# Kernel tuning notes

Hardware: AMD Instinct MI355X
Metric: run time of the kernel (lower is better)

Reference implementation:

```python
import jax, jax.numpy as jnp
import numpy as np

B = 65536; D1 = 64; D2 = 64; DC = 128; K = 8; DFF = 1024
NPP = 3 * K - 1                      # 23 params per output dim (non-adaptive)
MIN_BIN = 0.1; MIN_DERIV = 1e-3; ALPHA = 2.0
DEFAULT = 3.0; DL = -DEFAULT; DD = 2 * DEFAULT; MIN_DELTA = MIN_BIN * K
SHIFT = float(np.log(np.e - 1.0))
SHIFT_DX = float(np.log(np.exp(DD - MIN_DELTA) - 1.0))
EPS = 1e-6


def setup_inputs() -> dict:
    key = jax.random.key(0)
    ks = jax.random.split(key, 8)
    x1 = jax.random.normal(ks[0], (B, D1), dtype=jnp.float32)
    x2 = jax.random.normal(ks[1], (B, D2), dtype=jnp.float32)
    context = jax.random.normal(ks[2], (B, DC), dtype=jnp.float32)
    mask1 = jnp.ones((B, D1), dtype=jnp.float32)
    din = 2 * D1 + DC
    W0 = jax.random.normal(ks[3], (din, DFF), dtype=jnp.float32) / np.sqrt(din)
    b0 = jnp.zeros((DFF,), jnp.float32)
    W1 = jax.random.normal(ks[4], (DFF, DFF), dtype=jnp.float32) / np.sqrt(DFF)
    b1 = jnp.zeros((DFF,), jnp.float32)
    W2 = jax.random.normal(ks[5], (DFF, DFF), dtype=jnp.float32) / np.sqrt(DFF)
    b2 = jnp.zeros((DFF,), jnp.float32)
    W3 = jax.random.normal(ks[6], (DFF, NPP * D2), dtype=jnp.float32) / np.sqrt(DFF)
    b3 = jnp.zeros((NPP * D2,), jnp.float32)
    return dict(x1=x1, x2=x2, context=context, mask1=mask1,
                W0=W0, b0=b0, W1=W1, b1=b1, W2=W2, b2=b2, W3=W3, b3=b3)


def _rq_forward(x1, x2, context, mask1, W0, b0, W1, b1, W2, b2, W3, b3):
    # --- conditioner MLP: input = concat(x1, mask1, context) ---
    h = jnp.concatenate([x1, mask1, context], axis=-1)
    h = jax.nn.relu(h @ W0 + b0)
    h = jax.nn.relu(h @ W1 + b1)
    h = jax.nn.relu(h @ W2 + b2)
    params = (h @ W3 + b3).reshape(x1.shape[0], D2, NPP)  # [B, D2, 23]

    w_raw = params[..., :K]
    h_raw = params[..., K:2 * K]
    d_raw = params[..., 2 * K:3 * K - 1]
    zeros = jnp.zeros(params.shape[:-1] + (1,), params.dtype)  # non-adaptive raw params

    # --- _constrain ---
    log_weight = ALPHA * jnp.tanh(zeros / ALPHA)          # -> 0
    weight = jnp.exp(log_weight)                          # -> 1
    bias = ALPHA * jnp.tanh(zeros / ALPHA)                # -> 0
    derivs = MIN_DERIV + jax.nn.softplus(d_raw + SHIFT)
    derivs = jnp.concatenate([weight, derivs, weight], axis=-1)  # [B, D2, K+1]
    left = DL + DD * jnp.tanh(zeros / DD)                 # -> -3
    delta_x = MIN_DELTA + jax.nn.softplus(zeros + SHIFT_DX)
    right = left + delta_x                                # -> +3
    bottom = weight * left + bias
    top = weight * right + bias

    w = jax.nn.softmax(w_raw, axis=-1)
    w = MIN_BIN + (1.0 - MIN_BIN * K) * w
    cw = jnp.pad(jnp.cumsum(w, axis=-1), ((0, 0), (0, 0), (1, 0)))
    cw = (right - left) * cw + left                       # cumwidths [B, D2, K+1]
    hh = jax.nn.softmax(h_raw, axis=-1)
    hh = MIN_BIN + (1.0 - MIN_BIN * K) * hh
    ch = jnp.pad(jnp.cumsum(hh, axis=-1), ((0, 0), (0, 0), (1, 0)))
    ch = (top - bottom) * ch + bottom                     # cumheights [B, D2, K+1]

    widths = cw[..., 1:] - cw[..., :-1]
    heights = ch[..., 1:] - ch[..., :-1]

    # --- bin search (searchsorted right=True on bumped cumwidths) ---
    bumped = jnp.concatenate([cw[..., :-1], cw[..., -1:] + EPS], axis=-1)
    idx = jnp.clip(jnp.sum(bumped <= x2[..., None], axis=-1) - 1, 0, K - 1)[..., None]

    gat = lambda t: jnp.take_along_axis(t, idx, axis=-1)[..., 0]
    x_k = gat(cw); x_kd = gat(widths)
    y_k = gat(ch); y_kd = gat(heights)
    s_k = gat(heights / widths)
    d0 = gat(derivs); d1 = gat(derivs[..., 1:])

    # --- forward rational-quadratic spline ---
    xi = (x2 - x_k) / x_kd
    xi1m = xi * (1.0 - xi)
    alpha_k = y_kd * (s_k * xi ** 2 + d0 * xi1m)
    beta_k = s_k + (d1 + d0 - 2.0 * s_k) * xi1m
    z_sp = y_k + alpha_k / jnp.maximum(beta_k, 1e-8)
    num = s_k ** 2 * (d1 * xi ** 2 + 2.0 * s_k * xi1m + d0 * (1.0 - xi) ** 2)
    ld_sp = jnp.log(jnp.maximum(num, 1e-8)) - 2.0 * jnp.log(jnp.maximum(beta_k, 1e-8))

    # --- affine tails ---
    lw = log_weight[..., 0]; bs = bias[..., 0]
    z_af = jnp.exp(lw) * x2 + bs
    ld_af = jnp.broadcast_to(lw, x2.shape)

    l2 = jnp.broadcast_to(left[..., 0], x2.shape)
    r2 = jnp.broadcast_to(right[..., 0], x2.shape)
    inside = (l2 <= x2) & (x2 < r2)
    z2 = jnp.where(inside, z_sp, z_af)
    ld = jnp.where(inside, ld_sp, ld_af)
    return z2, ld.sum(-1)


def reference(x1, x2, context, mask1, W0, b0, W1, b1, W2, b2, W3, b3):
    return _rq_forward(x1, x2, context, mask1, W0, b0, W1, b1, W2, b2, W3, b3)
```

## Files before the change

kernel.cpp:

```cpp
#include <hip/hip_runtime.h>


typedef __bf16 bf16_t;
typedef __bf16 bf16x8 __attribute__((ext_vector_type(8)));
typedef float f32x4 __attribute__((ext_vector_type(4)));

#define GLOAD_LDS16(g, l)                                               \
  __builtin_amdgcn_global_load_lds(                                     \
      (const __attribute__((address_space(1))) void*)(g),               \
      (__attribute__((address_space(3))) void*)(l), 16, 0, 0)

__device__ __forceinline__ void xcd_remap(int& bx, int& by) {
  const int gx = gridDim.x;
  const int nwg = gx * gridDim.y;
  const int id = blockIdx.y * gx + blockIdx.x;
  const int nid = (id & 7) * (nwg >> 3) + (id >> 3);
  bx = nid % gx;
  by = nid / gx;
}

__global__ __launch_bounds__(256) void transpose_w(
    const float* __restrict__ W, bf16_t* __restrict__ Wt,
    int K, int N, int Npad) {
  __shared__ float tile[64][65];
  const int kt = blockIdx.x * 64;
  const int nt = blockIdx.y * 64;
  const int r4 = threadIdx.x >> 6;
  const int c = threadIdx.x & 63;
#pragma unroll
  for (int i = 0; i < 16; i++) {
    int r = i * 4 + r4;
    int gn = nt + c;
    tile[r][c] = (gn < N) ? W[(size_t)(kt + r) * N + gn] : 0.0f;
  }
  __syncthreads();
#pragma unroll
  for (int i = 0; i < 16; i++) {
    int r = i * 4 + r4;
    Wt[(size_t)(nt + r) * K + kt + c] = (bf16_t)tile[c][r];
  }
}

__global__ __launch_bounds__(256) void transpose_w3p(
    const float* __restrict__ W3, bf16_t* __restrict__ Wt) {
  __shared__ float tile[64][65];
  const int kt = blockIdx.x * 64;
  const int nt = blockIdx.y * 64;
  const int r4 = threadIdx.x >> 6;
  const int c = threadIdx.x & 63;
  const int np = nt + c;
  const int d = np / 24, p = np % 24;
#pragma unroll
  for (int i = 0; i < 16; i++) {
    int r = i * 4 + r4;
    tile[r][c] = (p < 23) ? W3[(size_t)(kt + r) * 1472 + d * 23 + p] : 0.0f;
  }
  __syncthreads();
#pragma unroll
  for (int i = 0; i < 16; i++) {
    int r = i * 4 + r4;
    Wt[(size_t)(nt + r) * 1024 + kt + c] = (bf16_t)tile[c][r];
  }
}

__global__ __launch_bounds__(256) void prep_b3(const float* __restrict__ b3,
                                               float* __restrict__ b3p) {
  int t = blockIdx.x * 256 + threadIdx.x;
  if (t < 1536) {
    int d = t / 24, p = t % 24;
    b3p[t] = (p < 23) ? b3[d * 23 + p] : 0.0f;
  }
}

__global__ __launch_bounds__(256) void build_x(
    const float* __restrict__ x1, const float* __restrict__ mask1,
    const float* __restrict__ ctx, bf16_t* __restrict__ X,
    float* __restrict__ ld_out, int boff) {
  int idx = blockIdx.x * 256 + threadIdx.x;
  int bl = idx >> 8;
  int c = idx & 255;
  size_t b = (size_t)(boff + bl);
  float v;
  if (c < 64)       v = x1[b * 64 + c];
  else if (c < 128) v = mask1[b * 64 + (c - 64)];
  else              v = ctx[b * 128 + (c - 128)];
  X[(size_t)bl * 256 + c] = (bf16_t)v;
  if (c == 0) ld_out[b] = 0.0f;
}

__global__ __launch_bounds__(512, 4) void gemm_bt(
    const bf16_t* __restrict__ A, const bf16_t* __restrict__ Bt,
    const float* __restrict__ bias, bf16_t* __restrict__ Cout, int N, int K) {
  __shared__ __align__(16) bf16_t As[2][128 * 32];
  __shared__ __align__(16) bf16_t Bs[2][256 * 32];
  const int tid = threadIdx.x;
  const int w = tid >> 6;
  const int lane = tid & 63;
  int bx, by;
  xcd_remap(bx, by);
  const int m0 = by * 128;
  const int n0 = bx * 256;
  const int wm = (w & 1) * 64;
  const int wn = (w >> 1) * 64;
  const int lrow = lane & 15;
  const int quad = lane >> 4;

  const bf16_t* gA;
  {
    const int byteoff = (w << 10) + lane * 16;
    const int row = byteoff >> 6;
    const int qs = ((byteoff >> 4) & 3) ^ ((row >> 1) & 3);
    gA = A + (size_t)(m0 + row) * K + qs * 8;
  }
  const bf16_t* gB0;
  const bf16_t* gB1;
  {
    int byteoff = (w << 10) + lane * 16;
    int row = byteoff >> 6;
    int qs = ((byteoff >> 4) & 3) ^ ((row >> 1) & 3);
    gB0 = Bt + (size_t)(n0 + row) * K + qs * 8;
    byteoff = ((w + 8) << 10) + lane * 16;
    row = byteoff >> 6;
    qs = ((byteoff >> 4) & 3) ^ ((row >> 1) & 3);
    gB1 = Bt + (size_t)(n0 + row) * K + qs * 8;
  }
  bf16_t* const dA0 = &As[0][0] + w * 512;
  bf16_t* const dB0 = &Bs[0][0] + w * 512;
  bf16_t* const dB1 = &Bs[0][0] + (w + 8) * 512;

  int offA[4], offB[4];
#pragma unroll
  for (int i = 0; i < 4; i++) {
    const int rowA = wm + i * 16 + lrow;
    offA[i] = rowA * 32 + (quad ^ ((rowA >> 1) & 3)) * 8;
    const int rowB = wn + i * 16 + lrow;
    offB[i] = rowB * 32 + (quad ^ ((rowB >> 1) & 3)) * 8;
  }

  f32x4 acc[4][4];
#pragma unroll
  for (int i = 0; i < 4; i++)
#pragma unroll
    for (int j = 0; j < 4; j++) acc[i][j] = (f32x4){0.f, 0.f, 0.f, 0.f};

  const int nPair = K >> 6;
  for (int kp = 0; kp < nPair; kp++) {
    GLOAD_LDS16(gA, dA0);
    GLOAD_LDS16(gA + 32, dA0 + 4096);
    GLOAD_LDS16(gB0, dB0);
    GLOAD_LDS16(gB0 + 32, dB0 + 8192);
    GLOAD_LDS16(gB1, dB1);
    GLOAD_LDS16(gB1 + 32, dB1 + 8192);
    gA += 64;
    gB0 += 64;
    gB1 += 64;
    __syncthreads();
#pragma unroll
    for (int h = 0; h < 2; h++) {
      bf16x8 af[4], bfr[4];
#pragma unroll
      for (int i = 0; i < 4; i++)
        af[i] = *(const bf16x8*)(&As[0][0] + h * 4096 + offA[i]);
#pragma unroll
      for (int j = 0; j < 4; j++)
        bfr[j] = *(const bf16x8*)(&Bs[0][0] + h * 8192 + offB[j]);
#pragma unroll
      for (int i = 0; i < 4; i++)
#pragma unroll
        for (int j = 0; j < 4; j++)
          acc[i][j] = __builtin_amdgcn_mfma_f32_16x16x32_bf16(
              af[i], bfr[j], acc[i][j], 0, 0, 0);
    }
    __syncthreads();
  }

  float bv[4];
#pragma unroll
  for (int j = 0; j < 4; j++) bv[j] = bias[n0 + wn + j * 16 + lrow];
#pragma unroll
  for (int i = 0; i < 4; i++) {
    int rbase = m0 + wm + i * 16 + quad * 4;
#pragma unroll
    for (int j = 0; j < 4; j++) {
      int col = n0 + wn + j * 16 + lrow;
#pragma unroll
      for (int r = 0; r < 4; r++) {
        float v = fmaxf(acc[i][j][r] + bv[j], 0.0f);
        Cout[(size_t)(rbase + r) * N + col] = (bf16_t)v;
      }
    }
  }
}

__global__ __launch_bounds__(512, 4) void gemm_rq_fused(
    const bf16_t* __restrict__ A, const bf16_t* __restrict__ Bt,
    const float* __restrict__ b3p, const float* __restrict__ x2,
    float* __restrict__ z_out, float* __restrict__ ld_out,
    int boff, int K) {
  union alignas(16) SM {
    struct { bf16_t As[2][128 * 32]; bf16_t Bs[2][192 * 32]; } s;
    bf16_t Pt[128 * 200];
  };
  __shared__ SM sm;
  const int tid = threadIdx.x;
  const int w = tid >> 6;
  const int lane = tid & 63;
  int bx, by;
  xcd_remap(bx, by);
  const int m0 = by * 128;
  const int n0 = bx * 192;
  const int wm = (w & 1) * 64;
  const int wn = (w >> 1) * 48;
  const int lrow = lane & 15;
  const int quad = lane >> 4;

  bf16_t* const smB = &sm.s.As[0][0];

  const bf16_t* gA;
  {
    const int byteoff = (w << 10) + lane * 16;
    const int row = byteoff >> 6;
    const int qs = ((byteoff >> 4) & 3) ^ ((row >> 1) & 3);
    gA = A + (size_t)(m0 + row) * K + qs * 8;
  }
  const bf16_t* gB0;
  const bf16_t* gB1;
  {
    int byteoff = (w << 10) + lane * 16;
    int row = byteoff >> 6;
    int qs = ((byteoff >> 4) & 3) ^ ((row >> 1) & 3);
    gB0 = Bt + (size_t)(n0 + row) * K + qs * 8;
    const int c1 = (w & 3) + 8;
    byteoff = (c1 << 10) + lane * 16;
    row = byteoff >> 6;
    qs = ((byteoff >> 4) & 3) ^ ((row >> 1) & 3);
    gB1 = Bt + (size_t)(n0 + row) * K + qs * 8;
  }
  bf16_t* const dA0 = smB + w * 512;
  bf16_t* const dB0 = smB + 8192 + w * 512;
  bf16_t* const dB1 = smB + 8192 + ((w & 3) + 8) * 512;

  int offA[4], offB3[3];
#pragma unroll
  for (int i = 0; i < 4; i++) {
    const int rowA = wm + i * 16 + lrow;
    offA[i] = rowA * 32 + (quad ^ ((rowA >> 1) & 3)) * 8;
  }
#pragma unroll
  for (int j = 0; j < 3; j++) {
    const int rowB = wn + j * 16 + lrow;
    offB3[j] = rowB * 32 + (quad ^ ((rowB >> 1) & 3)) * 8;
  }

  f32x4 acc[4][3];
#pragma unroll
  for (int i = 0; i < 4; i++)
#pragma unroll
    for (int j = 0; j < 3; j++) acc[i][j] = (f32x4){0.f, 0.f, 0.f, 0.f};

  const int nPair = K >> 6;
  for (int kp = 0; kp < nPair; kp++) {
    GLOAD_LDS16(gA, dA0);
    GLOAD_LDS16(gA + 32, dA0 + 4096);
    GLOAD_LDS16(gB0, dB0);
    GLOAD_LDS16(gB0 + 32, dB0 + 6144);
    if (w < 4) {
      GLOAD_LDS16(gB1, dB1);
      GLOAD_LDS16(gB1 + 32, dB1 + 6144);
      gB1 += 64;
    }
    gA += 64;
    gB0 += 64;
    __syncthreads();
#pragma unroll
    for (int h = 0; h < 2; h++) {
      bf16x8 af[4], bfr[3];
#pragma unroll
      for (int i = 0; i < 4; i++)
        af[i] = *(const bf16x8*)(smB + h * 4096 + offA[i]);
#pragma unroll
      for (int j = 0; j < 3; j++)
        bfr[j] = *(const bf16x8*)(smB + 8192 + h * 6144 + offB3[j]);
#pragma unroll
      for (int i = 0; i < 4; i++)
#pragma unroll
        for (int j = 0; j < 3; j++)
          acc[i][j] = __builtin_amdgcn_mfma_f32_16x16x32_bf16(
              af[i], bfr[j], acc[i][j], 0, 0, 0);
    }
    __syncthreads();
  }

  float bv[3];
#pragma unroll
  for (int j = 0; j < 3; j++) bv[j] = b3p[n0 + wn + j * 16 + lrow];
#pragma unroll
  for (int i = 0; i < 4; i++) {
    const int rbase = wm + i * 16 + quad * 4;
#pragma unroll
    for (int j = 0; j < 3; j++) {
      const int col = wn + j * 16 + lrow;
#pragma unroll
      for (int r = 0; r < 4; r++)
        sm.Pt[(rbase + r) * 200 + col] = (bf16_t)(acc[i][j][r] + bv[j]);
    }
  }
  __syncthreads();

  const float SHIFT = 0.54132485f;
  const float SHIFT_DX = 5.1944682f;
  const float left = -3.0f;
  const float delta_x = 0.8f + log1pf(expf(SHIFT_DX));
  const float right = left + delta_x;
  const float scale = delta_x;
  const int dloc = tid & 7;
  const int dg = bx * 8 + dloc;

#pragma unroll
  for (int rr = 0; rr < 2; rr++) {
    const int row = (tid >> 3) + rr * 64;
    const bf16_t* pr = sm.Pt + row * 200 + dloc * 24;
    const size_t bg = (size_t)(boff + m0 + row);
    const float x = x2[bg * 64 + dg];

    bf16x8 v0 = *(const bf16x8*)(pr);
    bf16x8 v1 = *(const bf16x8*)(pr + 8);
    bf16x8 v2 = *(const bf16x8*)(pr + 16);
    float pv[24];
#pragma unroll
    for (int j = 0; j < 8; j++) pv[j] = (float)v0[j];
#pragma unroll
    for (int j = 0; j < 8; j++) pv[8 + j] = (float)v1[j];
#pragma unroll
    for (int j = 0; j < 8; j++) pv[16 + j] = (float)v2[j];

    float mw = pv[0];
#pragma unroll
    for (int j = 1; j < 8; j++) mw = fmaxf(mw, pv[j]);
    float ew[8], swv = 0.f;
#pragma unroll
    for (int j = 0; j < 8; j++) { ew[j] = expf(pv[j] - mw); swv += ew[j]; }
    float invw = 1.0f / swv;
    float cw[9];
    cw[0] = left;
    float cum = 0.f;
#pragma unroll
    for (int j = 0; j < 8; j++) {
      cum += 0.1f + 0.2f * ew[j] * invw;
      cw[j + 1] = left + scale * cum;
    }
    float mh = pv[8];
#pragma unroll
    for (int j = 9; j < 16; j++) mh = fmaxf(mh, pv[j]);
    float eh[8], shv = 0.f;
#pragma unroll
    for (int j = 0; j < 8; j++) { eh[j] = expf(pv[8 + j] - mh); shv += eh[j]; }
    float invh = 1.0f / shv;
    float chh[9];
    chh[0] = left;
    float cumh = 0.f;
#pragma unroll
    for (int j = 0; j < 8; j++) {
      cumh += 0.1f + 0.2f * eh[j] * invh;
      chh[j + 1] = left + scale * cumh;
    }
    float dv[9];
    dv[0] = 1.0f;
    dv[8] = 1.0f;
#pragma unroll
    for (int j = 0; j < 7; j++) {
      float v = pv[16 + j] + SHIFT;
      dv[j + 1] = 0.001f + ((v > 20.f) ? v : log1pf(expf(v)));
    }
    int cnt = 0;
#pragma unroll
    for (int j = 0; j < 8; j++) cnt += (cw[j] <= x) ? 1 : 0;
    cnt += ((cw[8] + 1e-6f) <= x) ? 1 : 0;
    int idx = cnt - 1;
    idx = idx < 0 ? 0 : (idx > 7 ? 7 : idx);
    float x_k = cw[0], x_k1 = cw[1], y_k = chh[0], y_k1 = chh[1];
    float d0v = dv[0], d1v = dv[1];
#pragma unroll
    for (int j = 1; j < 8; j++) {
      bool s = (idx == j);
      x_k = s ? cw[j] : x_k;
      x_k1 = s ? cw[j + 1] : x_k1;
      y_k = s ? chh[j] : y_k;
      y_k1 = s ? chh[j + 1] : y_k1;
      d0v = s ? dv[j] : d0v;
      d1v = s ? dv[j + 1] : d1v;
    }
    float x_kd = x_k1 - x_k;
    float y_kd = y_k1 - y_k;
    float s_k = y_kd / x_kd;
    float xi = (x - x_k) / x_kd;
    float xi1m = xi * (1.f - xi);
    float alpha_k = y_kd * (s_k * xi * xi + d0v * xi1m);
    float beta_k = s_k + (d1v + d0v - 2.f * s_k) * xi1m;
    float z_sp = y_k + alpha_k / fmaxf(beta_k, 1e-8f);
    float oxi = 1.f - xi;
    float num = s_k * s_k * (d1v * xi * xi + 2.f * s_k * xi1m + d0v * oxi * oxi);
    float ld_sp = logf(fmaxf(num, 1e-8f)) - 2.f * logf(fmaxf(beta_k, 1e-8f));

    bool inside = (left <= x) && (x < right);
    z_out[bg * 64 + dg] = inside ? z_sp : x;
    float ldv = inside ? ld_sp : 0.f;
    ldv += __shfl_xor(ldv, 1);
    ldv += __shfl_xor(ldv, 2);
    ldv += __shfl_xor(ldv, 4);
    if (dloc == 0) atomicAdd(&ld_out[bg], ldv);
  }
}

extern "C" void kernel_launch(void* const* d_in, const int* in_sizes, int n_in,
                              void* d_out, int out_size, void* d_ws,
                              size_t ws_size, hipStream_t stream) {
  const float* x1 = (const float*)d_in[0];
  const float* x2 = (const float*)d_in[1];
  const float* ctx = (const float*)d_in[2];
  const float* mask1 = (const float*)d_in[3];
  const float* W0 = (const float*)d_in[4];
  const float* b0 = (const float*)d_in[5];
  const float* W1 = (const float*)d_in[6];
  const float* b1 = (const float*)d_in[7];
  const float* W2 = (const float*)d_in[8];
  const float* b2 = (const float*)d_in[9];
  const float* W3 = (const float*)d_in[10];
  const float* b3 = (const float*)d_in[11];
  float* out = (float*)d_out;

  const int B = 65536;
  char* ws = (char*)d_ws;

  bf16_t* Wt0 = (bf16_t*)ws;
  bf16_t* Wt1 = (bf16_t*)(ws + 524288);
  bf16_t* Wt2 = (bf16_t*)(ws + 524288 + 2097152);
  bf16_t* Wt3 = (bf16_t*)(ws + 524288 + 2 * 2097152);
  float* b3p = (float*)(ws + 524288 + 2 * 2097152 + 3145728);
  const size_t wend = 524288 + 2 * 2097152 + 3145728 + 8192;

  int C = 4;
  if (wend + (size_t)B * 4096 <= ws_size) C = 1;
  else if (wend + (size_t)(B / 2) * 4096 <= ws_size) C = 2;
  const int Bc = B / C;
  bf16_t* HA = (bf16_t*)(ws + wend);
  char* R = ws + wend + (size_t)Bc * 2048;
  bf16_t* X = (bf16_t*)R;
  bf16_t* HB = (bf16_t*)R;
  float* ld_out = out + (size_t)B * 64;

  transpose_w<<<dim3(4, 16), 256, 0, stream>>>(W0, Wt0, 256, 1024, 1024);
  transpose_w<<<dim3(16, 16), 256, 0, stream>>>(W1, Wt1, 1024, 1024, 1024);
  transpose_w<<<dim3(16, 16), 256, 0, stream>>>(W2, Wt2, 1024, 1024, 1024);
  transpose_w3p<<<dim3(16, 24), 256, 0, stream>>>(W3, Wt3);
  prep_b3<<<6, 256, 0, stream>>>(b3, b3p);

  for (int c = 0; c < C; c++) {
    const int boff = c * Bc;
    build_x<<<Bc, 256, 0, stream>>>(x1, mask1, ctx, X, ld_out, boff);
    gemm_bt<<<dim3(4, Bc / 128), 512, 0, stream>>>(X, Wt0, b0, HA, 1024, 256);
    gemm_bt<<<dim3(4, Bc / 128), 512, 0, stream>>>(HA, Wt1, b1, HB, 1024, 1024);
    gemm_bt<<<dim3(4, Bc / 128), 512, 0, stream>>>(HB, Wt2, b2, HA, 1024, 1024);
    gemm_rq_fused<<<dim3(8, Bc / 128), 512, 0, stream>>>(
        HA, Wt3, b3p, x2, out, ld_out, boff, 1024);
  }
}
```

Baseline: 812.9 us.

## Triple-buffer LDS in GEMM with async global-to-LDS prefetch pipeline

Replaces the synchronous load-then-compute loop, which issued both K-halves and waited on two barriers per iteration, with a three-stage ring of K=32 LDS buffers. Loads for step t+2 are issued while step t is computed, and explicit vmcnt waits plus a single barrier per step keep the stages in order. The goal is to hide global memory latency behind MFMA work. In exchange, LDS use per block rises from 48KB to 72KB, which may cut occupancy below the 4 blocks requested in launch bounds.

```diff
diff --git a/kernel.cpp b/kernel.cpp
--- a/kernel.cpp
+++ b/kernel.cpp
@@ -9,6 +9,9 @@
   __builtin_amdgcn_global_load_lds(                                     \
       (const __attribute__((address_space(1))) void*)(g),               \
       (__attribute__((address_space(3))) void*)(l), 16, 0, 0)
+
+#define WAITVM(N) asm volatile("s_waitcnt vmcnt(" #N ")" ::: "memory")
+#define SBAR() __builtin_amdgcn_s_barrier()
 
 __device__ __forceinline__ void xcd_remap(int& bx, int& by) {
   const int gx = gridDim.x;
@@ -91,8 +94,8 @@
 __global__ __launch_bounds__(512, 4) void gemm_bt(
     const bf16_t* __restrict__ A, const bf16_t* __restrict__ Bt,
     const float* __restrict__ bias, bf16_t* __restrict__ Cout, int N, int K) {
-  __shared__ __align__(16) bf16_t As[2][128 * 32];
-  __shared__ __align__(16) bf16_t Bs[2][256 * 32];
+  __shared__ __align__(16) bf16_t As[3][128 * 32];
+  __shared__ __align__(16) bf16_t Bs[3][256 * 32];
   const int tid = threadIdx.x;
   const int w = tid >> 6;
   const int lane = tid & 63;
@@ -124,9 +127,6 @@
     qs = ((byteoff >> 4) & 3) ^ ((row >> 1) & 3);
     gB1 = Bt + (size_t)(n0 + row) * K + qs * 8;
   }
-  bf16_t* const dA0 = &As[0][0] + w * 512;
-  bf16_t* const dB0 = &Bs[0][0] + w * 512;
-  bf16_t* const dB1 = &Bs[0][0] + (w + 8) * 512;
 
   int offA[4], offB[4];
 #pragma unroll
@@ -143,36 +143,40 @@
 #pragma unroll
     for (int j = 0; j < 4; j++) acc[i][j] = (f32x4){0.f, 0.f, 0.f, 0.f};
 
-  const int nPair = K >> 6;
-  for (int kp = 0; kp < nPair; kp++) {
-    GLOAD_LDS16(gA, dA0);
-    GLOAD_LDS16(gA + 32, dA0 + 4096);
-    GLOAD_LDS16(gB0, dB0);
-    GLOAD_LDS16(gB0 + 32, dB0 + 8192);
-    GLOAD_LDS16(gB1, dB1);
-    GLOAD_LDS16(gB1 + 32, dB1 + 8192);
-    gA += 64;
-    gB0 += 64;
-    gB1 += 64;
-    __syncthreads();
-#pragma unroll
-    for (int h = 0; h < 2; h++) {
-      bf16x8 af[4], bfr[4];
-#pragma unroll
-      for (int i = 0; i < 4; i++)
-        af[i] = *(const bf16x8*)(&As[0][0] + h * 4096 + offA[i]);
+#define MID_STAGE(BUF)                                                  \
+  do {                                                                  \
+    GLOAD_LDS16(gA, &As[BUF][0] + w * 512);                             \
+    GLOAD_LDS16(gB0, &Bs[BUF][0] + w * 512);                            \
+    GLOAD_LDS16(gB1, &Bs[BUF][0] + (w + 8) * 512);                      \
+    gA += 32; gB0 += 32; gB1 += 32;                                     \
+  } while (0)
+
+  const int nt = K >> 5;
+  MID_STAGE(0);
+  MID_STAGE(1);
+  int cur = 0;
+  int stg = 2;
+  for (int t = 0; t < nt; t++) {
+    if (t + 1 < nt) WAITVM(3); else WAITVM(0);
+    SBAR();
+    if (t + 2 < nt) MID_STAGE(stg);
+    bf16x8 af[4], bfr[4];
+#pragma unroll
+    for (int i = 0; i < 4; i++)
+      af[i] = *(const bf16x8*)(&As[cur][0] + offA[i]);
+#pragma unroll
+    for (int j = 0; j < 4; j++)
+      bfr[j] = *(const bf16x8*)(&Bs[cur][0] + offB[j]);
+#pragma unroll
+    for (int i = 0; i < 4; i++)
 #pragma unroll
       for (int j = 0; j < 4; j++)
-        bfr[j] = *(const bf16x8*)(&Bs[0][0] + h * 8192 + offB[j]);
-#pragma unroll
-      for (int i = 0; i < 4; i++)
-#pragma unroll
-        for (int j = 0; j < 4; j++)
-          acc[i][j] = __builtin_amdgcn_mfma_f32_16x16x32_bf16(
-              af[i], bfr[j], acc[i][j], 0, 0, 0);
-    }
-    __syncthreads();
-  }
+        acc[i][j] = __builtin_amdgcn_mfma_f32_16x16x32_bf16(
+            af[i], bfr[j], acc[i][j], 0, 0, 0);
+    cur = (cur == 2) ? 0 : cur + 1;
+    stg = (stg == 2) ? 0 : stg + 1;
+  }
+#undef MID_STAGE
 
   float bv[4];
 #pragma unroll
```

New measurement: 838.4 us. 1.03x slower.
